# Optimization experiments

Hardware: AMD Instinct MI355X
Metric: run time of the kernel (lower is better)

## Reference

```python
import jax, jax.numpy as jnp
import numpy as np


def setup_inputs() -> dict:
    key = jax.random.key(0)
    k1, k2, k3, k4 = jax.random.split(key, 4)
    B, S, D = 8, 2048, 1024
    query = jax.random.normal(k1, (B, S, D), dtype=jnp.float32)
    key_t = jax.random.normal(k2, (B, S, D), dtype=jnp.float32)
    value = jax.random.normal(k3, (B, S, D), dtype=jnp.float32)
    # Dense(embed_dim) kernel/bias; NOTE: source (buggy but faithful) uses the
    # SAME query_linear weights for q, k, and v projections.
    Wq = jax.random.normal(k4, (D, D), dtype=jnp.float32) * (1.0 / np.sqrt(D))
    bq = jnp.zeros((D,), dtype=jnp.float32)
    return {"query": query, "key": key_t, "value": value, "Wq": Wq, "bq": bq}


def reference(query, key, value, Wq, bq):
    # All three projections use query_linear, matching the original source.
    q = query @ Wq + bq            # [B, S, D]
    k = key @ Wq + bq              # [B, S, D]
    v = value @ Wq + bq            # [B, S, D]
    dim_key = jnp.asarray(k.shape[-1], dtype=jnp.float32)
    logits = jnp.einsum('bqd,bkd->bqk', q, k) / jnp.sqrt(dim_key)  # [B, S, S]
    weights = jax.nn.softmax(logits, axis=-1)
    # dropout_rate = 0.0 / inference: dropout is identity
    out = jnp.einsum('bqk,bkd->bqd', weights, v)  # [B, S, D]
    return out
```

## Files before the change

kernel.cpp:

```cpp
#include <hip/hip_runtime.h>
#include <hip/hip_bf16.h>
#include <stdint.h>

typedef __attribute__((ext_vector_type(8))) short short8;
typedef __attribute__((ext_vector_type(4))) float f32x4;
typedef __attribute__((ext_vector_type(8))) unsigned short ushort8v;

__device__ __forceinline__ unsigned short f2bf(float f) {
  union { float f; uint32_t u; } v; v.f = f;
  uint32_t u = v.u;
  u += 0x7fffu + ((u >> 16) & 1u);
  return (unsigned short)(u >> 16);
}
__device__ __forceinline__ unsigned short f2h(float f) {
  union { _Float16 h; unsigned short u; } v; v.h = (_Float16)f; return v.u;
}
__device__ __forceinline__ float h2f(unsigned short u) {
  union { _Float16 h; unsigned short u; } v; v.u = u; return (float)v.h;
}

typedef const __attribute__((address_space(1))) unsigned int* gas_ptr;
typedef __attribute__((address_space(3))) unsigned int* las_ptr;

__device__ __forceinline__ void async16(const unsigned short* g, unsigned short* l) {
  __builtin_amdgcn_global_load_lds((gas_ptr)g, (las_ptr)l, 16, 0, 0);
}

#define BM 128
#define BN 128
#define BK 64

template<int EPI>
__global__ __launch_bounds__(256) void gemm_bf16(
    const unsigned short* __restrict__ Abase,
    const unsigned short* __restrict__ Bbase,
    void* __restrict__ Cbase, const float* __restrict__ bias, float scale,
    int lda, int ldb, int ldc, int K,
    long long sA, long long sB, long long sC)
{
  __shared__ __align__(16) unsigned short As[BM * BK];
  __shared__ __align__(16) unsigned short Bs[BN * BK];

  const int tid  = threadIdx.x;
  const int z    = blockIdx.z;
  const int m0   = blockIdx.x * BM;
  const int n0   = blockIdx.y * BN;
  const int wave = tid >> 6;
  const int lane = tid & 63;
  const int l16  = lane & 15;
  const int quad = lane >> 4;
  const int wm   = (wave >> 1) * 64;
  const int wn   = (wave & 1) * 64;

  const unsigned short* A = Abase + (size_t)z * (size_t)sA;
  const unsigned short* B = Bbase + (size_t)z * (size_t)sB;

  f32x4 acc[4][4] = {};

  const int nk = K / BK;
  for (int kt = 0; kt < nk; ++kt) {
    const int k0 = kt * BK;
    #pragma unroll
    for (int j = 0; j < 4; ++j) {
      const int i  = j * 256 + tid;
      const int r  = i >> 3;
      const int s  = i & 7;
      const int jc = s ^ (r & 7);
      unsigned short* ldst_a = As + (size_t)(j * 256 + wave * 64) * 8;
      unsigned short* ldst_b = Bs + (size_t)(j * 256 + wave * 64) * 8;
      async16(A + (size_t)(m0 + r) * lda + k0 + jc * 8, ldst_a);
      async16(B + (size_t)(n0 + r) * ldb + k0 + jc * 8, ldst_b);
    }
    __syncthreads();

    #pragma unroll
    for (int h = 0; h < 2; ++h) {
      short8 af[4], bfr[4];
      #pragma unroll
      for (int mt = 0; mt < 4; ++mt) {
        const int R = wm + mt * 16 + l16;
        const int slot = (h * 4 + quad) ^ (R & 7);
        af[mt] = *(const short8*)&As[R * BK + slot * 8];
      }
      #pragma unroll
      for (int nt = 0; nt < 4; ++nt) {
        const int R = wn + nt * 16 + l16;
        const int slot = (h * 4 + quad) ^ (R & 7);
        bfr[nt] = *(const short8*)&Bs[R * BK + slot * 8];
      }
      #pragma unroll
      for (int mt = 0; mt < 4; ++mt)
        #pragma unroll
        for (int nt = 0; nt < 4; ++nt)
          acc[mt][nt] = __builtin_amdgcn_mfma_f32_16x16x32_bf16(
              af[mt], bfr[nt], acc[mt][nt], 0, 0, 0);
    }
    __syncthreads();
  }

  #pragma unroll
  for (int mt = 0; mt < 4; ++mt) {
    #pragma unroll
    for (int nt = 0; nt < 4; ++nt) {
      #pragma unroll
      for (int r = 0; r < 4; ++r) {
        const int Rg = m0 + wm + mt * 16 + quad * 4 + r;
        const int Cg = n0 + wn + nt * 16 + l16;
        const size_t off = (size_t)z * (size_t)sC + (size_t)Rg * ldc + Cg;
        const float val = acc[mt][nt][r];
        if (EPI == 0) {
          ((unsigned short*)Cbase)[off] = f2bf(val + bias[Cg]);
        } else if (EPI == 1) {
          ((unsigned short*)Cbase)[off] = f2h(val * scale);
        } else {
          ((float*)Cbase)[off] = val * scale;
        }
      }
    }
  }
}

__global__ __launch_bounds__(256) void cvt3_bf16(
    const float* __restrict__ a, const float* __restrict__ b,
    const float* __restrict__ c,
    unsigned short* __restrict__ oa, unsigned short* __restrict__ ob,
    unsigned short* __restrict__ oc)
{
  const float* src = blockIdx.z == 0 ? a : (blockIdx.z == 1 ? b : c);
  unsigned short* dst = blockIdx.z == 0 ? oa : (blockIdx.z == 1 ? ob : oc);
  const size_t base = ((size_t)blockIdx.x * 256 + threadIdx.x) * 8;
  const float4 t0 = *(const float4*)(src + base);
  const float4 t1 = *(const float4*)(src + base + 4);
  ushort8v h;
  h[0] = f2bf(t0.x); h[1] = f2bf(t0.y); h[2] = f2bf(t0.z); h[3] = f2bf(t0.w);
  h[4] = f2bf(t1.x); h[5] = f2bf(t1.y); h[6] = f2bf(t1.z); h[7] = f2bf(t1.w);
  *(ushort8v*)(dst + base) = h;
}

__global__ __launch_bounds__(256) void transpose_w(
    const float* __restrict__ W, unsigned short* __restrict__ Wt)
{
  __shared__ float tile[64][65];
  const int k0 = blockIdx.x * 64;
  const int n0 = blockIdx.y * 64;
  #pragma unroll
  for (int i = 0; i < 16; ++i) {
    int lin = threadIdx.x + i * 256;
    int r = lin >> 6, c = lin & 63;
    tile[r][c] = W[(size_t)(k0 + r) * 1024 + n0 + c];
  }
  __syncthreads();
  #pragma unroll
  for (int i = 0; i < 16; ++i) {
    int lin = threadIdx.x + i * 256;
    int r = lin >> 6, c = lin & 63;
    Wt[(size_t)(n0 + r) * 1024 + k0 + c] = f2bf(tile[c][r]);
  }
}

__global__ __launch_bounds__(256) void transpose_v(
    const unsigned short* __restrict__ V, unsigned short* __restrict__ VT)
{
  __shared__ unsigned short tile[64][66];
  const int b  = blockIdx.z;
  const int s0 = blockIdx.x * 64;
  const int d0 = blockIdx.y * 64;
  const unsigned short* Vb  = V  + (size_t)b * 2048 * 1024;
  unsigned short*       VTb = VT + (size_t)b * 1024 * 2048;
  #pragma unroll
  for (int i = 0; i < 16; ++i) {
    int lin = threadIdx.x + i * 256;
    int r = lin >> 6, c = lin & 63;
    tile[r][c] = Vb[(size_t)(s0 + r) * 1024 + d0 + c];
  }
  __syncthreads();
  #pragma unroll
  for (int i = 0; i < 16; ++i) {
    int lin = threadIdx.x + i * 256;
    int r = lin >> 6, c = lin & 63;
    VTb[(size_t)(d0 + r) * 2048 + s0 + c] = tile[c][r];
  }
}

__global__ __launch_bounds__(256) void softmax_rows(
    const unsigned short* __restrict__ Lh, unsigned short* __restrict__ P)
{
  const int row  = blockIdx.x;
  const unsigned short* pin = Lh + (size_t)row * 2048;
  unsigned short*       pout = P + (size_t)row * 2048;
  const int tid  = threadIdx.x;
  const int lane = tid & 63;
  const int wave = tid >> 6;

  const ushort8v h = ((const ushort8v*)pin)[tid];
  float x[8];
  #pragma unroll
  for (int e = 0; e < 8; ++e) x[e] = h2f(h[e]);

  float mx = x[0];
  #pragma unroll
  for (int e = 1; e < 8; ++e) mx = fmaxf(mx, x[e]);
  #pragma unroll
  for (int o = 32; o > 0; o >>= 1) mx = fmaxf(mx, __shfl_xor(mx, o));
  __shared__ float redm[4];
  if (lane == 0) redm[wave] = mx;
  __syncthreads();
  mx = fmaxf(fmaxf(redm[0], redm[1]), fmaxf(redm[2], redm[3]));

  float s = 0.f;
  #pragma unroll
  for (int e = 0; e < 8; ++e) { x[e] = __expf(x[e] - mx); s += x[e]; }
  #pragma unroll
  for (int o = 32; o > 0; o >>= 1) s += __shfl_xor(s, o);
  __shared__ float reds[4];
  if (lane == 0) reds[wave] = s;
  __syncthreads();
  s = reds[0] + reds[1] + reds[2] + reds[3];

  const float inv = 1.0f / s;
  ushort8v o8;
  #pragma unroll
  for (int e = 0; e < 8; ++e) o8[e] = f2bf(x[e] * inv);
  ((ushort8v*)pout)[tid] = o8;
}

extern "C" void kernel_launch(void* const* d_in, const int* in_sizes, int n_in,
                              void* d_out, int out_size, void* d_ws, size_t ws_size,
                              hipStream_t stream)
{
  const float* query = (const float*)d_in[0];
  const float* key   = (const float*)d_in[1];
  const float* value = (const float*)d_in[2];
  const float* Wq    = (const float*)d_in[3];
  const float* bq    = (const float*)d_in[4];
  float* out = (float*)d_out;

  char* ws = (char*)d_ws;
  unsigned short* Wt  = (unsigned short*)(ws);
  unsigned short* Xq  = (unsigned short*)(ws + ((size_t)2   << 20));
  unsigned short* Xk  = (unsigned short*)(ws + ((size_t)34  << 20));
  unsigned short* Xv  = (unsigned short*)(ws + ((size_t)66  << 20));
  unsigned short* q   = (unsigned short*)(ws + ((size_t)98  << 20));
  unsigned short* v   = (unsigned short*)(ws + ((size_t)162 << 20));
  unsigned short* vT  = (unsigned short*)(ws + ((size_t)2   << 20));
  unsigned short* lgH = (unsigned short*)(ws + ((size_t)34  << 20));
  unsigned short* P   = (unsigned short*)(ws + ((size_t)98  << 20));

  transpose_w<<<dim3(16, 16, 1), 256, 0, stream>>>(Wq, Wt);
  cvt3_bf16<<<dim3(8192, 1, 3), 256, 0, stream>>>(query, key, value, Xq, Xk, Xv);

  gemm_bf16<0><<<dim3(16384 / BM, 1024 / BN, 3), 256, 0, stream>>>(
      Xq, Wt, q, bq, 1.0f, 1024, 1024, 1024, 1024,
      (long long)16384 * 1024, 0, (long long)16384 * 1024);

  transpose_v<<<dim3(32, 16, 8), 256, 0, stream>>>(v, vT);

  gemm_bf16<1><<<dim3(16, 16, 8), 256, 0, stream>>>(q, q + (size_t)32 * 1024 * 1024 / 2,
      lgH, nullptr, 0.03125f, 1024, 1024, 2048, 1024,
      (long long)2048 * 1024, (long long)2048 * 1024, (long long)2048 * 2048);

  softmax_rows<<<dim3(8 * 2048, 1, 1), 256, 0, stream>>>(lgH, P);

  gemm_bf16<2><<<dim3(16, 8, 8), 256, 0, stream>>>(P, vT, out, nullptr, 1.0f,
      2048, 2048, 1024, 2048,
      (long long)2048 * 2048, (long long)1024 * 2048, (long long)2048 * 1024);
}
```

Before: 573.8 us.

## Replace GEMM with 256x256 double-buffered pipelined kernel and XCD-aware block swizzle

Rewrites the shared bf16 GEMM as a 256x256 tile kernel with 512 threads and 8 waves, each wave computing a 128x64 sub-tile. The K loop is split into half-tiles with double-buffered LDS and async global-to-LDS prefetch two stages ahead. Fine-grained barriers and s_setprio interleave MFMA with loads. A flattened grid with a modulo-8 swizzle groups tiles per XCD for L2 reuse. The goal is to hide load latency and raise arithmetic intensity, at the cost of much more LDS (128KB), more registers and fewer blocks for the smaller GEMMs.

```diff
diff --git a/kernel.cpp b/kernel.cpp
--- a/kernel.cpp
+++ b/kernel.cpp
@@ -26,90 +26,152 @@
   __builtin_amdgcn_global_load_lds((gas_ptr)g, (las_ptr)l, 16, 0, 0);
 }
 
-#define BM 128
-#define BN 128
+#define FENCE() asm volatile("" ::: "memory")
+#define BARRIER() do { FENCE(); __builtin_amdgcn_s_barrier(); FENCE(); } while (0)
+
+#define BM 256
+#define BN 256
 #define BK 64
+#define RGN 8192
 
 template<int EPI>
-__global__ __launch_bounds__(256) void gemm_bf16(
+__global__ __launch_bounds__(512, 2) void gemm256(
     const unsigned short* __restrict__ Abase,
     const unsigned short* __restrict__ Bbase,
     void* __restrict__ Cbase, const float* __restrict__ bias, float scale,
-    int lda, int ldb, int ldc, int K,
+    int lda, int ldb, int ldc, int K, int mtiles, int ntiles,
     long long sA, long long sB, long long sC)
 {
-  __shared__ __align__(16) unsigned short As[BM * BK];
-  __shared__ __align__(16) unsigned short Bs[BN * BK];
+  __shared__ __align__(16) unsigned short lds[8 * RGN];
 
   const int tid  = threadIdx.x;
-  const int z    = blockIdx.z;
-  const int m0   = blockIdx.x * BM;
-  const int n0   = blockIdx.y * BN;
+  const int nwg  = (int)gridDim.x;
+  const int flat = (int)blockIdx.x;
+  const int swz = (flat & 7) * (nwg >> 3) + (flat >> 3);
+  const int per = mtiles * ntiles;
+  const int z   = swz / per;
+  const int rm  = swz - z * per;
+  const int mb  = rm / ntiles;
+  const int nb  = rm - mb * ntiles;
+  const int m0  = mb * BM;
+  const int n0  = nb * BN;
+
   const int wave = tid >> 6;
   const int lane = tid & 63;
   const int l16  = lane & 15;
   const int quad = lane >> 4;
-  const int wm   = (wave >> 1) * 64;
-  const int wn   = (wave & 1) * 64;
+  const int wm   = wave >> 2;
+  const int wn   = wave & 3;
 
   const unsigned short* A = Abase + (size_t)z * (size_t)sA;
   const unsigned short* B = Bbase + (size_t)z * (size_t)sB;
 
-  f32x4 acc[4][4] = {};
-
-  const int nk = K / BK;
-  for (int kt = 0; kt < nk; ++kt) {
-    const int k0 = kt * BK;
+  const int RA   = wm * 128 + l16;
+  const int RB   = wn * 64  + l16;
+  const int offA = RA * 32 + (quad ^ ((RA >> 1) & 3)) * 8;
+  const int offB = RB * 32 + (quad ^ ((RB >> 1) & 3)) * 8;
+
+  f32x4 acc[8][4] = {};
+
+  const int nt = K / BK;
+
+  auto stageA = [&](int kt, int h, int b) {
+    unsigned short* rgn = lds + (size_t)(b * 4 + h) * RGN;
+    #pragma unroll
+    for (int i = 0; i < 2; ++i) {
+      const int c  = i * 512 + tid;
+      const int r  = c >> 2;
+      const int s  = c & 3;
+      const int sc = s ^ ((r >> 1) & 3);
+      async16(A + (size_t)(m0 + r) * lda + kt * 64 + h * 32 + sc * 8,
+              rgn + (size_t)(i * 512 + wave * 64) * 8);
+    }
+  };
+  auto stageB = [&](int kt, int h, int b) {
+    unsigned short* rgn = lds + (size_t)(b * 4 + 2 + h) * RGN;
+    #pragma unroll
+    for (int i = 0; i < 2; ++i) {
+      const int c  = i * 512 + tid;
+      const int r  = c >> 2;
+      const int s  = c & 3;
+      const int sc = s ^ ((r >> 1) & 3);
+      async16(B + (size_t)(n0 + r) * ldb + kt * 64 + h * 32 + sc * 8,
+              rgn + (size_t)(i * 512 + wave * 64) * 8);
+    }
+  };
+
+  stageA(0, 0, 0); stageB(0, 0, 0); stageA(0, 1, 0); stageB(0, 1, 0);
+  stageA(1, 0, 1); stageB(1, 0, 1); stageA(1, 1, 1);
+  asm volatile("s_waitcnt vmcnt(6)" ::: "memory");
+  BARRIER();
+
+#define MFMA_QUAD(AF, BF, J0)                                                   \
+  do {                                                                          \
+    __builtin_amdgcn_s_setprio(1);                                              \
+    _Pragma("unroll")                                                           \
+    for (int mt = 0; mt < 8; ++mt) {                                            \
+      acc[mt][J0]     = __builtin_amdgcn_mfma_f32_16x16x32_bf16(                \
+          AF[mt], BF[J0],     acc[mt][J0],     0, 0, 0);                        \
+      acc[mt][J0 + 1] = __builtin_amdgcn_mfma_f32_16x16x32_bf16(                \
+          AF[mt], BF[J0 + 1], acc[mt][J0 + 1], 0, 0, 0);                        \
+    }                                                                           \
+    __builtin_amdgcn_s_setprio(0);                                              \
+  } while (0)
+
+  int cur = 0;
+  for (int t = 0; t < nt; ++t, cur ^= 1) {
+    const unsigned short* Ah0 = lds + (size_t)(cur * 4 + 0) * RGN;
+    const unsigned short* Ah1 = Ah0 + RGN;
+    const unsigned short* Bh0 = lds + (size_t)(cur * 4 + 2) * RGN;
+    const unsigned short* Bh1 = Bh0 + RGN;
+
+    short8 a0[8], a1[8], b0[4], b1[4];
+
+    #pragma unroll
+    for (int mt = 0; mt < 8; ++mt) a0[mt] = *(const short8*)&Ah0[offA + mt * 512];
+    #pragma unroll
+    for (int j = 0; j < 4; ++j)    b0[j]  = *(const short8*)&Bh0[offB + j * 512];
+    if (t + 1 < nt) stageB(t + 1, 1, cur ^ 1);
+    BARRIER();
+    MFMA_QUAD(a0, b0, 0);
+    BARRIER();
+
+    #pragma unroll
+    for (int mt = 0; mt < 8; ++mt) a1[mt] = *(const short8*)&Ah1[offA + mt * 512];
+    if (t + 2 < nt) stageA(t + 2, 0, cur);
+    BARRIER();
+    MFMA_QUAD(a0, b0, 2);
+    BARRIER();
+
+    #pragma unroll
+    for (int j = 0; j < 4; ++j) b1[j] = *(const short8*)&Bh1[offB + j * 512];
+    if (t + 2 < nt) stageB(t + 2, 0, cur);
+    BARRIER();
+    MFMA_QUAD(a1, b1, 0);
+    BARRIER();
+
+    if (t + 2 < nt) stageA(t + 2, 1, cur);
+    if (t < nt - 2)       asm volatile("s_waitcnt vmcnt(6)" ::: "memory");
+    else if (t == nt - 2) asm volatile("s_waitcnt vmcnt(0)" ::: "memory");
+    BARRIER();
+    MFMA_QUAD(a1, b1, 2);
+    BARRIER();
+  }
+
+  #pragma unroll
+  for (int mt = 0; mt < 8; ++mt) {
+    const int Rg = m0 + wm * 128 + mt * 16 + quad * 4;
     #pragma unroll
     for (int j = 0; j < 4; ++j) {
-      const int i  = j * 256 + tid;
-      const int r  = i >> 3;
-      const int s  = i & 7;
-      const int jc = s ^ (r & 7);
-      unsigned short* ldst_a = As + (size_t)(j * 256 + wave * 64) * 8;
-      unsigned short* ldst_b = Bs + (size_t)(j * 256 + wave * 64) * 8;
-      async16(A + (size_t)(m0 + r) * lda + k0 + jc * 8, ldst_a);
-      async16(B + (size_t)(n0 + r) * ldb + k0 + jc * 8, ldst_b);
-    }
-    __syncthreads();
-
-    #pragma unroll
-    for (int h = 0; h < 2; ++h) {
-      short8 af[4], bfr[4];
-      #pragma unroll
-      for (int mt = 0; mt < 4; ++mt) {
-        const int R = wm + mt * 16 + l16;
-        const int slot = (h * 4 + quad) ^ (R & 7);
-        af[mt] = *(const short8*)&As[R * BK + slot * 8];
-      }
-      #pragma unroll
-      for (int nt = 0; nt < 4; ++nt) {
-        const int R = wn + nt * 16 + l16;
-        const int slot = (h * 4 + quad) ^ (R & 7);
-        bfr[nt] = *(const short8*)&Bs[R * BK + slot * 8];
-      }
-      #pragma unroll
-      for (int mt = 0; mt < 4; ++mt)
-        #pragma unroll
-        for (int nt = 0; nt < 4; ++nt)
-          acc[mt][nt] = __builtin_amdgcn_mfma_f32_16x16x32_bf16(
-              af[mt], bfr[nt], acc[mt][nt], 0, 0, 0);
-    }
-    __syncthreads();
-  }
-
-  #pragma unroll
-  for (int mt = 0; mt < 4; ++mt) {
-    #pragma unroll
-    for (int nt = 0; nt < 4; ++nt) {
+      const int Cg = n0 + wn * 64 + j * 16 + l16;
+      float badd = 0.f;
+      if (EPI == 0) badd = bias[Cg];
       #pragma unroll
       for (int r = 0; r < 4; ++r) {
-        const int Rg = m0 + wm + mt * 16 + quad * 4 + r;
-        const int Cg = n0 + wn + nt * 16 + l16;
-        const size_t off = (size_t)z * (size_t)sC + (size_t)Rg * ldc + Cg;
-        const float val = acc[mt][nt][r];
+        const size_t off = (size_t)z * (size_t)sC + (size_t)(Rg + r) * ldc + Cg;
+        const float val = acc[mt][j][r];
         if (EPI == 0) {
-          ((unsigned short*)Cbase)[off] = f2bf(val + bias[Cg]);
+          ((unsigned short*)Cbase)[off] = f2bf(val + badd);
         } else if (EPI == 1) {
           ((unsigned short*)Cbase)[off] = f2h(val * scale);
         } else {
@@ -249,19 +311,20 @@
   transpose_w<<<dim3(16, 16, 1), 256, 0, stream>>>(Wq, Wt);
   cvt3_bf16<<<dim3(8192, 1, 3), 256, 0, stream>>>(query, key, value, Xq, Xk, Xv);
 
-  gemm_bf16<0><<<dim3(16384 / BM, 1024 / BN, 3), 256, 0, stream>>>(
-      Xq, Wt, q, bq, 1.0f, 1024, 1024, 1024, 1024,
+  gemm256<0><<<dim3(768, 1, 1), 512, 0, stream>>>(
+      Xq, Wt, q, bq, 1.0f, 1024, 1024, 1024, 1024, 64, 4,
       (long long)16384 * 1024, 0, (long long)16384 * 1024);
 
   transpose_v<<<dim3(32, 16, 8), 256, 0, stream>>>(v, vT);
 
-  gemm_bf16<1><<<dim3(16, 16, 8), 256, 0, stream>>>(q, q + (size_t)32 * 1024 * 1024 / 2,
-      lgH, nullptr, 0.03125f, 1024, 1024, 2048, 1024,
+  gemm256<1><<<dim3(512, 1, 1), 512, 0, stream>>>(
+      q, q + (size_t)32 * 1024 * 1024 / 2, lgH, nullptr, 0.03125f,
+      1024, 1024, 2048, 1024, 8, 8,
       (long long)2048 * 1024, (long long)2048 * 1024, (long long)2048 * 2048);
 
   softmax_rows<<<dim3(8 * 2048, 1, 1), 256, 0, stream>>>(lgH, P);
 
-  gemm_bf16<2><<<dim3(16, 8, 8), 256, 0, stream>>>(P, vT, out, nullptr, 1.0f,
-      2048, 2048, 1024, 2048,
+  gemm256<2><<<dim3(256, 1, 1), 512, 0, stream>>>(
+      P, vT, out, nullptr, 1.0f, 2048, 2048, 1024, 2048, 8, 4,
       (long long)2048 * 2048, (long long)1024 * 2048, (long long)2048 * 1024);
 }
```

Result: faster. 505.6 us (-11.9%).
